# Optimization experiments

Measured on AMD Instinct MI355X. Metric: run time of the kernel, lower is better.

## Reference

```python
import jax, jax.numpy as jnp
import numpy as np

N, E, E_D, EN_D, H = 50000, 200000, 16, 64, 32


def setup_inputs() -> dict:
    key = jax.random.key(0)
    ks = jax.random.split(key, 12)
    x = jax.random.normal(ks[0], (N, H), dtype=jnp.float32)
    edge_data = jax.random.normal(ks[1], (E, E_D), dtype=jnp.float32)
    edges = jax.random.randint(ks[2], (E, 2), 0, N, dtype=jnp.int32)
    # edge_net params: Linear(e_d->en_d), Linear(en_d->h*h)
    W1 = jax.random.normal(ks[3], (EN_D, E_D), dtype=jnp.float32) / np.sqrt(E_D)
    b1 = jax.random.normal(ks[4], (EN_D,), dtype=jnp.float32) * 0.01
    W2 = jax.random.normal(ks[5], (H * H, EN_D), dtype=jnp.float32) / np.sqrt(EN_D)
    b2 = jax.random.normal(ks[6], (H * H,), dtype=jnp.float32) * 0.01
    # GRUCell(input=2*h, hidden=h) params (torch layout: [3h, in], gates r,z,n)
    W_ih = jax.random.normal(ks[7], (3 * H, 2 * H), dtype=jnp.float32) / np.sqrt(2 * H)
    W_hh = jax.random.normal(ks[8], (3 * H, H), dtype=jnp.float32) / np.sqrt(H)
    b_ih = jax.random.normal(ks[9], (3 * H,), dtype=jnp.float32) * 0.01
    b_hh = jax.random.normal(ks[10], (3 * H,), dtype=jnp.float32) * 0.01
    return {"x": x, "edge_data": edge_data, "edges": edges, "T": 8,
            "W1": W1, "b1": b1, "W2": W2, "b2": b2,
            "W_ih": W_ih, "W_hh": W_hh, "b_ih": b_ih, "b_hh": b_hh}


def _gru_cell(inp, h, W_ih, W_hh, b_ih, b_hh):
    gi = inp @ W_ih.T + b_ih   # [N, 3h]
    gh = h @ W_hh.T + b_hh     # [N, 3h]
    i_r, i_z, i_n = jnp.split(gi, 3, axis=1)
    h_r, h_z, h_n = jnp.split(gh, 3, axis=1)
    r = jax.nn.sigmoid(i_r + h_r)
    z = jax.nn.sigmoid(i_z + h_z)
    n = jnp.tanh(i_n + r * h_n)
    return (1.0 - z) * n + z * h


def reference(x, edge_data, edges, T, W1, b1, W2, b2, W_ih, W_hh, b_ih, b_hh):
    h = x.shape[1]
    # per-edge message matrices A_e = edge_net(edge_data_e): [E, h, h]
    hid = jax.nn.relu(edge_data @ W1.T + b1)
    A = jax.nn.relu(hid @ W2.T + b2).reshape(-1, h, h)
    src, dst = edges[:, 0], edges[:, 1]
    # message src is ALWAYS edges[e,0]; message added to both endpoints,
    # only once when src == dst (faithful to the v/e_id loop in the original).
    not_self = (src != dst)[:, None].astype(x.dtype)
    for _ in range(T):
        msg = jnp.einsum('eij,ej->ei', A, x[src])            # [E, h]
        m = jnp.zeros_like(x).at[src].add(msg).at[dst].add(msg * not_self)
        x = _gru_cell(jnp.concatenate([x, m], axis=1), x, W_ih, W_hh, b_ih, b_hh)
    return x
```

## Files before the change

### kernel.cpp

```cpp
#include <hip/hip_runtime.h>
#include <stdint.h>

#define N_NODES 50000
#define N_EDGES 200000
#define H 32
#define T_STEPS 8
#define NGROUPS (N_EDGES / 64)
#define SCAN_B 196

typedef __attribute__((ext_vector_type(4))) float v4f;
typedef __attribute__((ext_vector_type(8))) _Float16 h8;

#define LO_SCALE 4096.0f
#define LO_DESCALE 2.44140625e-4f

__device__ __forceinline__ uint32_t packh2(_Float16 a, _Float16 b) {
  return (uint32_t)__builtin_bit_cast(unsigned short, a) |
         ((uint32_t)__builtin_bit_cast(unsigned short, b) << 16);
}

__global__ void w1pack_kernel(const float* __restrict__ W1, float* __restrict__ W1P) {
  int o = threadIdx.x + blockIdx.x * blockDim.x;
  int d = o >> 4, k = o & 15;
  W1P[k * 64 + d] = W1[o];
}

__global__ void hidb_kernel(const float* __restrict__ ed, const float* __restrict__ W1P,
                            const float* __restrict__ b1,
                            uint32_t* __restrict__ hidh, uint32_t* __restrict__ hidl) {
  int idx = blockIdx.x * blockDim.x + threadIdx.x;
  int e = idx >> 5, d2 = idx & 31;
  int d0 = d2 * 2;
  const float4* er = (const float4*)(ed + (size_t)e * 16);
  float2 bb = *(const float2*)(b1 + d0);
  float a0 = bb.x, a1 = bb.y;
#pragma unroll
  for (int k = 0; k < 4; k++) {
    float4 h = er[k];
    float2 w0 = *(const float2*)(W1P + (4 * k + 0) * 64 + d0);
    float2 w1 = *(const float2*)(W1P + (4 * k + 1) * 64 + d0);
    float2 w2 = *(const float2*)(W1P + (4 * k + 2) * 64 + d0);
    float2 w3 = *(const float2*)(W1P + (4 * k + 3) * 64 + d0);
    a0 += h.x * w0.x + h.y * w1.x + h.z * w2.x + h.w * w3.x;
    a1 += h.x * w0.y + h.y * w1.y + h.z * w2.y + h.w * w3.y;
  }
  a0 = fmaxf(a0, 0.f);
  a1 = fmaxf(a1, 0.f);
  _Float16 h0 = (_Float16)a0, h1 = (_Float16)a1;
  _Float16 l0 = (_Float16)((a0 - (float)h0) * LO_SCALE);
  _Float16 l1 = (_Float16)((a1 - (float)h1) * LO_SCALE);
  hidh[idx] = packh2(h0, h1);
  hidl[idx] = packh2(l0, l1);
}

__global__ void w2pack_kernel(const float* __restrict__ W2,
                              uint32_t* __restrict__ W2Fh, uint32_t* __restrict__ W2Fl) {
  int o = blockIdx.x * blockDim.x + threadIdx.x;
  int c = o >> 8, u = o & 255;
  int lane = u >> 2, pr = u & 3;
  int mtg = c >> 1, kh = c & 1;
  int row = mtg * 16 + (lane & 15);
  int k = kh * 32 + (lane >> 4) * 8 + pr * 2;
  float v0 = W2[(size_t)row * 64 + k];
  float v1 = W2[(size_t)row * 64 + k + 1];
  _Float16 h0 = (_Float16)v0, h1 = (_Float16)v1;
  _Float16 l0 = (_Float16)((v0 - (float)h0) * LO_SCALE);
  _Float16 l1 = (_Float16)((v1 - (float)h1) * LO_SCALE);
  W2Fh[o] = packh2(h0, h1);
  W2Fl[o] = packh2(l0, l1);
}

__global__ void zero_cur_kernel(int* __restrict__ cur) {
  int i = blockIdx.x * blockDim.x + threadIdx.x;
  if (i < N_NODES) cur[i] = 0;
}
__global__ void count_kernel(const int* __restrict__ edges, int* __restrict__ cur) {
  int e = blockIdx.x * blockDim.x + threadIdx.x;
  if (e < N_EDGES) {
    int s = edges[2 * e], d = edges[2 * e + 1];
    atomicAdd(&cur[s], 1);
    if (d != s) atomicAdd(&cur[d], 1);
  }
}
__global__ __launch_bounds__(256) void bsum_kernel(const int* __restrict__ cur,
                                                   int* __restrict__ bsum) {
  __shared__ int s[256];
  int b = blockIdx.x, t = threadIdx.x;
  int idx = b * 256 + t;
  s[t] = (idx < N_NODES) ? cur[idx] : 0;
  __syncthreads();
  for (int d = 128; d > 0; d >>= 1) {
    if (t < d) s[t] += s[t + d];
    __syncthreads();
  }
  if (t == 0) bsum[b] = s[0];
}
__global__ __launch_bounds__(256) void bscan_kernel(const int* __restrict__ bsum,
                                                    int* __restrict__ bbase,
                                                    int* __restrict__ off) {
  __shared__ int s[256];
  int t = threadIdx.x;
  int v = (t < SCAN_B) ? bsum[t] : 0;
  s[t] = v;
  __syncthreads();
  for (int d = 1; d < 256; d <<= 1) {
    int u = (t >= d) ? s[t - d] : 0;
    __syncthreads();
    s[t] += u;
    __syncthreads();
  }
  if (t < SCAN_B) bbase[t] = s[t] - v;
  if (t == SCAN_B - 1) off[N_NODES] = s[t];
}
__global__ __launch_bounds__(256) void boff_kernel(const int* __restrict__ bbase,
                                                   int* __restrict__ cur,
                                                   int* __restrict__ off) {
  __shared__ int s[256];
  int b = blockIdx.x, t = threadIdx.x;
  int idx = b * 256 + t;
  int v = (idx < N_NODES) ? cur[idx] : 0;
  s[t] = v;
  __syncthreads();
  for (int d = 1; d < 256; d <<= 1) {
    int u = (t >= d) ? s[t - d] : 0;
    __syncthreads();
    s[t] += u;
    __syncthreads();
  }
  if (idx < N_NODES) {
    int ex = bbase[b] + s[t] - v;
    off[idx] = ex;
    cur[idx] = ex;
  }
}
__global__ void scatter_kernel(const int* __restrict__ edges, int* __restrict__ cur,
                               int* __restrict__ inc) {
  int e = blockIdx.x * blockDim.x + threadIdx.x;
  if (e < N_EDGES) {
    int s = edges[2 * e], d = edges[2 * e + 1];
    int p = atomicAdd(&cur[s], 1);
    inc[p] = e;
    if (d != s) {
      p = atomicAdd(&cur[d], 1);
      inc[p] = e;
    }
  }
}

typedef __attribute__((address_space(1))) const uint32_t gq_u32;
typedef __attribute__((address_space(3))) uint32_t lds_q_u32;
__device__ __forceinline__ void gload_lds16(const uint32_t* g, uint32_t* l) {
  __builtin_amdgcn_global_load_lds((gq_u32*)g, (lds_q_u32*)l, 16, 0, 0);
}

__device__ __forceinline__ void stage_eighth(const uint32_t* __restrict__ W2Fh,
                                             const uint32_t* __restrict__ W2Fl,
                                             uint32_t* bh, uint32_t* bl,
                                             int eighth, int wv, int lane) {
#pragma unroll
  for (int k = 0; k < 4; k++) {
    int ub = (wv * 4 + k) * 256;
    int u  = ub + lane * 4;
    gload_lds16(W2Fh + eighth * 4096 + u, bh + ub);
    gload_lds16(W2Fl + eighth * 4096 + u, bl + ub);
  }
}

template <int NS>
__device__ __forceinline__ void do_pass(
    const uint32_t* __restrict__ W2Fh, const uint32_t* __restrict__ W2Fl,
    uint32_t (*w2h)[4096], uint32_t (*w2l)[4096], const float* b2s,
    const h8 (&bh0)[NS], const h8 (&bh1)[NS],
    const h8 (&bl0)[NS], const h8 (&bl1)[NS],
    const v4f (&xv0)[NS], const v4f (&xv1)[NS], const int (&ee)[NS],
    float* __restrict__ msg, int wv, int lane, int kg, bool last) {
  int cb = 0;
  for (int s = 0; s < 8; ++s) {
    if (!(last && s == 7)) {
      stage_eighth(W2Fh, W2Fl, w2h[cb ^ 1], w2l[cb ^ 1], (s + 1) & 7, wv, lane);
    }
    int q = s >> 1, h = s & 1;
    const h8* sh = (const h8*)w2h[cb];
    const h8* sl = (const h8*)w2l[cb];
    const float* b2p = b2s + q * 256 + h * 128 + kg * 4;

    float sacc[NS][4];
#pragma unroll
    for (int mp2 = 0; mp2 < 4; mp2++) {
      float tacc[NS];
#pragma unroll
      for (int u = 0; u < NS; u++) tacc[u] = 0.f;
#pragma unroll
      for (int tp = 0; tp < 2; tp++) {
        int lm = 2 * mp2 + tp;
        h8 ah0 = sh[(size_t)(lm * 2 + 0) * 64 + lane];
        h8 ah1 = sh[(size_t)(lm * 2 + 1) * 64 + lane];
        h8 al0 = sl[(size_t)(lm * 2 + 0) * 64 + lane];
        h8 al1 = sl[(size_t)(lm * 2 + 1) * 64 + lane];
        v4f bias = *(const v4f*)(b2p + lm * 16);
#pragma unroll
        for (int u = 0; u < NS; u++) {
          v4f chi = bias;
          chi = __builtin_amdgcn_mfma_f32_16x16x32_f16(ah0, bh0[u], chi, 0, 0, 0);
          chi = __builtin_amdgcn_mfma_f32_16x16x32_f16(ah1, bh1[u], chi, 0, 0, 0);
          v4f clo = {0.f, 0.f, 0.f, 0.f};
          clo = __builtin_amdgcn_mfma_f32_16x16x32_f16(ah0, bl0[u], clo, 0, 0, 0);
          clo = __builtin_amdgcn_mfma_f32_16x16x32_f16(ah1, bl1[u], clo, 0, 0, 0);
          clo = __builtin_amdgcn_mfma_f32_16x16x32_f16(al0, bh0[u], clo, 0, 0, 0);
          clo = __builtin_amdgcn_mfma_f32_16x16x32_f16(al1, bh1[u], clo, 0, 0, 0);
          v4f xr = tp ? xv1[u] : xv0[u];
#pragma unroll
          for (int r = 0; r < 4; r++) {
            float av = fmaxf(fmaf(clo[r], LO_DESCALE, chi[r]), 0.f);
            tacc[u] = fmaf(av, xr[r], tacc[u]);
          }
        }
      }
#pragma unroll
      for (int u = 0; u < NS; u++) {
        float sv = tacc[u];
        sv += __shfl_xor(sv, 16, 64);
        sv += __shfl_xor(sv, 32, 64);
        sacc[u][mp2] = sv;
      }
    }
    if (lane < 16) {
#pragma unroll
      for (int u = 0; u < NS; u++) {
        v4f sv4 = {sacc[u][0], sacc[u][1], sacc[u][2], sacc[u][3]};
        *(v4f*)(msg + (size_t)ee[u] * 32 + q * 8 + h * 4) = sv4;
      }
    }
    __syncthreads();
    cb ^= 1;
  }
}

template <int NS>
__device__ __forceinline__ void load_sets(
    const uint32_t* __restrict__ hidh, const uint32_t* __restrict__ hidl,
    const float* __restrict__ x, const int* __restrict__ edges,
    int gbase, int wv, int el, int kg,
    h8 (&bh0)[NS], h8 (&bh1)[NS], h8 (&bl0)[NS], h8 (&bl1)[NS],
    v4f (&xv0)[NS], v4f (&xv1)[NS], int (&ee)[NS]) {
  const h8* hbh = (const h8*)hidh;
  const h8* hbl = (const h8*)hidl;
#pragma unroll
  for (int u = 0; u < NS; u++) {
    int e = (gbase + u) * 64 + wv * 16 + el;
    ee[u] = e;
    int src = edges[2 * e];
    bh0[u] = hbh[(size_t)e * 8 + kg];
    bh1[u] = hbh[(size_t)e * 8 + 4 + kg];
    bl0[u] = hbl[(size_t)e * 8 + kg];
    bl1[u] = hbl[(size_t)e * 8 + 4 + kg];
    xv0[u] = *(const v4f*)(x + (size_t)src * 32 + kg * 4);
    xv1[u] = *(const v4f*)(x + (size_t)src * 32 + 16 + kg * 4);
  }
}

__global__ __launch_bounds__(256, 2) void msg_kernel(
    const uint32_t* __restrict__ W2Fh, const uint32_t* __restrict__ W2Fl,
    const uint32_t* __restrict__ hidh, const uint32_t* __restrict__ hidl,
    const float* __restrict__ b2, const float* __restrict__ x,
    const int* __restrict__ edges, float* __restrict__ msg) {
  __shared__ uint32_t w2h[2][4096];
  __shared__ uint32_t w2l[2][4096];
  __shared__ float b2s[1024];
  int t = threadIdx.x;
  int bid = blockIdx.x;
  int gs = (int)(((long)bid * NGROUPS) >> 9);
  int ge = (int)(((long)(bid + 1) * NGROUPS) >> 9);
  int n = ge - gs;
  int wv = t >> 6, lane = t & 63;
  int el = lane & 15, kg = lane >> 4;

  for (int i = t; i < 1024; i += 256) b2s[i] = b2[i];
  stage_eighth(W2Fh, W2Fl, w2h[0], w2l[0], 0, wv, lane);

  h8 bh0[4], bh1[4], bl0[4], bl1[4];
  v4f xv0[4], xv1[4];
  int ee[4];
  load_sets<4>(hidh, hidl, x, edges, gs, wv, el, kg,
               bh0, bh1, bl0, bl1, xv0, xv1, ee);
  __syncthreads();

  do_pass<4>(W2Fh, W2Fl, w2h, w2l, b2s, bh0, bh1, bl0, bl1, xv0, xv1, ee,
             msg, wv, lane, kg, false);

  __builtin_amdgcn_sched_barrier(0);

  if (n == 6) {
    h8 cbh0[2], cbh1[2], cbl0[2], cbl1[2];
    v4f cxv0[2], cxv1[2];
    int cee[2];
    load_sets<2>(hidh, hidl, x, edges, gs + 4, wv, el, kg,
                 cbh0, cbh1, cbl0, cbl1, cxv0, cxv1, cee);
    do_pass<2>(W2Fh, W2Fl, w2h, w2l, b2s, cbh0, cbh1, cbl0, cbl1,
               cxv0, cxv1, cee, msg, wv, lane, kg, true);
  } else {
    h8 cbh0[3], cbh1[3], cbl0[3], cbl1[3];
    v4f cxv0[3], cxv1[3];
    int cee[3];
    load_sets<3>(hidh, hidl, x, edges, gs + 4, wv, el, kg,
                 cbh0, cbh1, cbl0, cbl1, cxv0, cxv1, cee);
    do_pass<3>(W2Fh, W2Fl, w2h, w2l, b2s, cbh0, cbh1, cbl0, cbl1,
               cxv0, cxv1, cee, msg, wv, lane, kg, true);
  }
}

__global__ __launch_bounds__(512) void node_kernel(
    float* __restrict__ x, const float* __restrict__ msg,
    const int* __restrict__ off, const int* __restrict__ inc,
    const float* __restrict__ W_ih, const float* __restrict__ W_hh,
    const float* __restrict__ b_ih, const float* __restrict__ b_hh) {
  __shared__ float wih[64 * 97];
  __shared__ float whh[32 * 97];
  __shared__ float xs[16][32], ms[16][32];
  int t = threadIdx.x;
  for (int p = t; p < 6144; p += 512) {
    int q = p >> 6, k = p & 63;
    wih[k * 97 + q] = W_ih[p];
  }
  for (int p = t; p < 3072; p += 512) {
    int q = p >> 5, k = p & 31;
    whh[k * 97 + q] = W_hh[p];
  }
  int slot = t >> 5, i = t & 31;
  int n = blockIdx.x * 16 + slot;
  float xv = x[(size_t)n * 32 + i];
  xs[slot][i] = xv;
  const float* msgq = msg + i;
  int s0 = off[n], s1 = off[n + 1];
  float a0 = 0.f, a1 = 0.f, a2 = 0.f, a3 = 0.f;
  float a4 = 0.f, a5 = 0.f, a6 = 0.f, a7 = 0.f;
  int k = s0;
  for (; k + 8 <= s1; k += 8) {
    int e0 = inc[k],     e1 = inc[k + 1], e2 = inc[k + 2], e3 = inc[k + 3];
    int e4 = inc[k + 4], e5 = inc[k + 5], e6 = inc[k + 6], e7 = inc[k + 7];
    a0 += msgq[(size_t)e0 * 32];
    a1 += msgq[(size_t)e1 * 32];
    a2 += msgq[(size_t)e2 * 32];
    a3 += msgq[(size_t)e3 * 32];
    a4 += msgq[(size_t)e4 * 32];
    a5 += msgq[(size_t)e5 * 32];
    a6 += msgq[(size_t)e6 * 32];
    a7 += msgq[(size_t)e7 * 32];
  }
  if (k + 4 <= s1) {
    int e0 = inc[k], e1 = inc[k + 1], e2 = inc[k + 2], e3 = inc[k + 3];
    a0 += msgq[(size_t)e0 * 32];
    a1 += msgq[(size_t)e1 * 32];
    a2 += msgq[(size_t)e2 * 32];
    a3 += msgq[(size_t)e3 * 32];
    k += 4;
  }
  for (; k < s1; k++) a0 += msgq[(size_t)inc[k] * 32];
  ms[slot][i] = ((a0 + a1) + (a2 + a3)) + ((a4 + a5) + (a6 + a7));
  __syncthreads();

  float gir = b_ih[i], giz = b_ih[32 + i], gin = b_ih[64 + i];
  float ghr = b_hh[i], ghz = b_hh[32 + i], ghn = b_hh[64 + i];
#pragma unroll 4
  for (int kk = 0; kk < 32; kk++) {
    float xk = xs[slot][kk];
    float mk = ms[slot][kk];
    const float* wa = &wih[kk * 97];
    const float* wb = &wih[(32 + kk) * 97];
    gir += xk * wa[i] + mk * wb[i];
    giz += xk * wa[32 + i] + mk * wb[32 + i];
    gin += xk * wa[64 + i] + mk * wb[64 + i];
    const float* hc = &whh[kk * 97];
    ghr += xk * hc[i];
    ghz += xk * hc[32 + i];
    ghn += xk * hc[64 + i];
  }
  float r = 1.f / (1.f + __expf(-(gir + ghr)));
  float z = 1.f / (1.f + __expf(-(giz + ghz)));
  float nn = tanhf(gin + r * ghn);
  x[(size_t)n * 32 + i] = (1.f - z) * nn + z * xv;
}

__global__ void copy4_kernel(float4* __restrict__ dst, const float4* __restrict__ src, int n4) {
  int i = blockIdx.x * blockDim.x + threadIdx.x;
  if (i < n4) dst[i] = src[i];
}

extern "C" void kernel_launch(void* const* d_in, const int* in_sizes, int n_in,
                              void* d_out, int out_size, void* d_ws, size_t ws_size,
                              hipStream_t stream) {
  const float* x_in      = (const float*)d_in[0];
  const float* edge_data = (const float*)d_in[1];
  const int*   edges     = (const int*)d_in[2];
  const float* W1   = (const float*)d_in[4];
  const float* b1   = (const float*)d_in[5];
  const float* W2   = (const float*)d_in[6];
  const float* b2   = (const float*)d_in[7];
  const float* W_ih = (const float*)d_in[8];
  const float* W_hh = (const float*)d_in[9];
  const float* b_ih = (const float*)d_in[10];
  const float* b_hh = (const float*)d_in[11];

  char* ws = (char*)d_ws;
  size_t o = 0;
  uint32_t* hidh = (uint32_t*)(ws + o); o += (size_t)N_EDGES * 64 * 2;
  uint32_t* hidl = (uint32_t*)(ws + o); o += (size_t)N_EDGES * 64 * 2;
  uint32_t* W2Fh = (uint32_t*)(ws + o); o += 32768u * 4;
  uint32_t* W2Fl = (uint32_t*)(ws + o); o += 32768u * 4;
  float*    W1P  = (float*)(ws + o);    o += 1024u * 4;
  int*      inc  = (int*)(ws + o);      o += (size_t)2 * N_EDGES * 4;
  int*      off  = (int*)(ws + o);      o += (size_t)(N_NODES + 4) * 4;
  int*      cur  = (int*)(ws + o);      o += (size_t)N_NODES * 4;
  int*      bsum = (int*)(ws + o);      o += (size_t)256 * 4;
  int*      bbase= (int*)(ws + o);      o += (size_t)256 * 4;
  float*    msg  = (float*)(ws + o);    o += (size_t)N_EDGES * 32 * 4;
  float*    x    = (float*)d_out;

  const int n4x = N_NODES * H / 4;
  copy4_kernel<<<(n4x + 255) / 256, 256, 0, stream>>>((float4*)x, (const float4*)x_in, n4x);
  w1pack_kernel<<<4, 256, 0, stream>>>(W1, W1P);
  hidb_kernel<<<N_EDGES * 32 / 256, 256, 0, stream>>>(edge_data, W1P, b1, hidh, hidl);
  w2pack_kernel<<<32768 / 256, 256, 0, stream>>>(W2, W2Fh, W2Fl);

  zero_cur_kernel<<<(N_NODES + 255) / 256, 256, 0, stream>>>(cur);
  count_kernel<<<(N_EDGES + 255) / 256, 256, 0, stream>>>(edges, cur);
  bsum_kernel<<<SCAN_B, 256, 0, stream>>>(cur, bsum);
  bscan_kernel<<<1, 256, 0, stream>>>(bsum, bbase, off);
  boff_kernel<<<SCAN_B, 256, 0, stream>>>(bbase, cur, off);
  scatter_kernel<<<(N_EDGES + 255) / 256, 256, 0, stream>>>(edges, cur, inc);

  for (int it = 0; it < T_STEPS; it++) {
    msg_kernel<<<512, 256, 0, stream>>>(W2Fh, W2Fl, hidh, hidl, b2, x, edges, msg);
    node_kernel<<<N_NODES / 16, 512, 0, stream>>>(x, msg, off, inc,
                                                  W_ih, W_hh, b_ih, b_hh);
  }
}
```

Measured before the change: 1.347 ms.

## Double msg_kernel grid and stage W2 in sixteenths with smaller LDS buffers

The message kernel now launches 1024 blocks instead of 512, so each block handles 3-4 edge groups in a single pass rather than two passes over 6-7 groups. The W2 weight staging is split into 16 smaller chunks, which halves the LDS double buffers. The first half of each output quad is held in registers until the second half is computed. The aim is more blocks, better occupancy and better load balance across CUs, at the cost of re-streaming the full W2 matrix once per block (twice as many total W2 reads) and twice as many barriers per pass.

```diff
diff --git a/kernel.cpp b/kernel.cpp
--- a/kernel.cpp
+++ b/kernel.cpp
@@ -7,6 +7,7 @@
 #define T_STEPS 8
 #define NGROUPS (N_EDGES / 64)
 #define SCAN_B 196
+#define MSG_GRID 1024
 
 typedef __attribute__((ext_vector_type(4))) float v4f;
 typedef __attribute__((ext_vector_type(8))) _Float16 h8;
@@ -153,51 +154,52 @@
   __builtin_amdgcn_global_load_lds((gq_u32*)g, (lds_q_u32*)l, 16, 0, 0);
 }
 
-__device__ __forceinline__ void stage_eighth(const uint32_t* __restrict__ W2Fh,
-                                             const uint32_t* __restrict__ W2Fl,
-                                             uint32_t* bh, uint32_t* bl,
-                                             int eighth, int wv, int lane) {
-#pragma unroll
-  for (int k = 0; k < 4; k++) {
-    int ub = (wv * 4 + k) * 256;
+__device__ __forceinline__ void stage_16th(const uint32_t* __restrict__ W2Fh,
+                                           const uint32_t* __restrict__ W2Fl,
+                                           uint32_t* bh, uint32_t* bl,
+                                           int s16, int wv, int lane) {
+#pragma unroll
+  for (int k = 0; k < 2; k++) {
+    int ub = (wv * 2 + k) * 256;
     int u  = ub + lane * 4;
-    gload_lds16(W2Fh + eighth * 4096 + u, bh + ub);
-    gload_lds16(W2Fl + eighth * 4096 + u, bl + ub);
+    gload_lds16(W2Fh + s16 * 2048 + u, bh + ub);
+    gload_lds16(W2Fl + s16 * 2048 + u, bl + ub);
   }
 }
 
 template <int NS>
 __device__ __forceinline__ void do_pass(
     const uint32_t* __restrict__ W2Fh, const uint32_t* __restrict__ W2Fl,
-    uint32_t (*w2h)[4096], uint32_t (*w2l)[4096], const float* b2s,
+    uint32_t (*w2h)[2048], uint32_t (*w2l)[2048], const float* b2s,
     const h8 (&bh0)[NS], const h8 (&bh1)[NS],
     const h8 (&bl0)[NS], const h8 (&bl1)[NS],
     const v4f (&xv0)[NS], const v4f (&xv1)[NS], const int (&ee)[NS],
-    float* __restrict__ msg, int wv, int lane, int kg, bool last) {
+    float* __restrict__ msg, int wv, int lane, int kg) {
   int cb = 0;
-  for (int s = 0; s < 8; ++s) {
-    if (!(last && s == 7)) {
-      stage_eighth(W2Fh, W2Fl, w2h[cb ^ 1], w2l[cb ^ 1], (s + 1) & 7, wv, lane);
+  float hold[NS][2];
+  for (int s = 0; s < 16; ++s) {
+    if (s < 15) {
+      stage_16th(W2Fh, W2Fl, w2h[cb ^ 1], w2l[cb ^ 1], s + 1, wv, lane);
     }
-    int q = s >> 1, h = s & 1;
+    int q = s >> 2, h = (s >> 1) & 1, half = s & 1;
     const h8* sh = (const h8*)w2h[cb];
     const h8* sl = (const h8*)w2l[cb];
-    const float* b2p = b2s + q * 256 + h * 128 + kg * 4;
-
-    float sacc[NS][4];
-#pragma unroll
-    for (int mp2 = 0; mp2 < 4; mp2++) {
+
+    float sacc[NS][2];
+#pragma unroll
+    for (int mp2 = 0; mp2 < 2; mp2++) {
       float tacc[NS];
 #pragma unroll
       for (int u = 0; u < NS; u++) tacc[u] = 0.f;
 #pragma unroll
       for (int tp = 0; tp < 2; tp++) {
-        int lm = 2 * mp2 + tp;
-        h8 ah0 = sh[(size_t)(lm * 2 + 0) * 64 + lane];
-        h8 ah1 = sh[(size_t)(lm * 2 + 1) * 64 + lane];
-        h8 al0 = sl[(size_t)(lm * 2 + 0) * 64 + lane];
-        h8 al1 = sl[(size_t)(lm * 2 + 1) * 64 + lane];
-        v4f bias = *(const v4f*)(b2p + lm * 16);
+        int lml = 2 * mp2 + tp;
+        h8 ah0 = sh[(size_t)(lml * 2 + 0) * 64 + lane];
+        h8 ah1 = sh[(size_t)(lml * 2 + 1) * 64 + lane];
+        h8 al0 = sl[(size_t)(lml * 2 + 0) * 64 + lane];
+        h8 al1 = sl[(size_t)(lml * 2 + 1) * 64 + lane];
+        int lm = half * 4 + lml;
+        v4f bias = *(const v4f*)(b2s + q * 256 + h * 128 + lm * 16 + kg * 4);
 #pragma unroll
         for (int u = 0; u < NS; u++) {
           v4f chi = bias;
@@ -224,10 +226,16 @@
         sacc[u][mp2] = sv;
       }
     }
-    if (lane < 16) {
+    if (half == 0) {
 #pragma unroll
       for (int u = 0; u < NS; u++) {
-        v4f sv4 = {sacc[u][0], sacc[u][1], sacc[u][2], sacc[u][3]};
+        hold[u][0] = sacc[u][0];
+        hold[u][1] = sacc[u][1];
+      }
+    } else if (lane < 16) {
+#pragma unroll
+      for (int u = 0; u < NS; u++) {
+        v4f sv4 = {hold[u][0], hold[u][1], sacc[u][0], sacc[u][1]};
         *(v4f*)(msg + (size_t)ee[u] * 32 + q * 8 + h * 4) = sv4;
       }
     }
@@ -264,48 +272,38 @@
     const uint32_t* __restrict__ hidh, const uint32_t* __restrict__ hidl,
     const float* __restrict__ b2, const float* __restrict__ x,
     const int* __restrict__ edges, float* __restrict__ msg) {
-  __shared__ uint32_t w2h[2][4096];
-  __shared__ uint32_t w2l[2][4096];
+  __shared__ uint32_t w2h[2][2048];
+  __shared__ uint32_t w2l[2][2048];
   __shared__ float b2s[1024];
   int t = threadIdx.x;
   int bid = blockIdx.x;
-  int gs = (int)(((long)bid * NGROUPS) >> 9);
-  int ge = (int)(((long)(bid + 1) * NGROUPS) >> 9);
+  int gs = (int)(((long)bid * NGROUPS) >> 10);
+  int ge = (int)(((long)(bid + 1) * NGROUPS) >> 10);
   int n = ge - gs;
   int wv = t >> 6, lane = t & 63;
   int el = lane & 15, kg = lane >> 4;
 
   for (int i = t; i < 1024; i += 256) b2s[i] = b2[i];
-  stage_eighth(W2Fh, W2Fl, w2h[0], w2l[0], 0, wv, lane);
-
-  h8 bh0[4], bh1[4], bl0[4], bl1[4];
-  v4f xv0[4], xv1[4];
-  int ee[4];
-  load_sets<4>(hidh, hidl, x, edges, gs, wv, el, kg,
-               bh0, bh1, bl0, bl1, xv0, xv1, ee);
-  __syncthreads();
-
-  do_pass<4>(W2Fh, W2Fl, w2h, w2l, b2s, bh0, bh1, bl0, bl1, xv0, xv1, ee,
-             msg, wv, lane, kg, false);
-
-  __builtin_amdgcn_sched_barrier(0);
-
-  if (n == 6) {
-    h8 cbh0[2], cbh1[2], cbl0[2], cbl1[2];
-    v4f cxv0[2], cxv1[2];
-    int cee[2];
-    load_sets<2>(hidh, hidl, x, edges, gs + 4, wv, el, kg,
-                 cbh0, cbh1, cbl0, cbl1, cxv0, cxv1, cee);
-    do_pass<2>(W2Fh, W2Fl, w2h, w2l, b2s, cbh0, cbh1, cbl0, cbl1,
-               cxv0, cxv1, cee, msg, wv, lane, kg, true);
+  stage_16th(W2Fh, W2Fl, w2h[0], w2l[0], 0, wv, lane);
+
+  if (n == 4) {
+    h8 bh0[4], bh1[4], bl0[4], bl1[4];
+    v4f xv0[4], xv1[4];
+    int ee[4];
+    load_sets<4>(hidh, hidl, x, edges, gs, wv, el, kg,
+                 bh0, bh1, bl0, bl1, xv0, xv1, ee);
+    __syncthreads();
+    do_pass<4>(W2Fh, W2Fl, w2h, w2l, b2s, bh0, bh1, bl0, bl1, xv0, xv1, ee,
+               msg, wv, lane, kg);
   } else {
-    h8 cbh0[3], cbh1[3], cbl0[3], cbl1[3];
-    v4f cxv0[3], cxv1[3];
-    int cee[3];
-    load_sets<3>(hidh, hidl, x, edges, gs + 4, wv, el, kg,
-                 cbh0, cbh1, cbl0, cbl1, cxv0, cxv1, cee);
-    do_pass<3>(W2Fh, W2Fl, w2h, w2l, b2s, cbh0, cbh1, cbl0, cbl1,
-               cxv0, cxv1, cee, msg, wv, lane, kg, true);
+    h8 bh0[3], bh1[3], bl0[3], bl1[3];
+    v4f xv0[3], xv1[3];
+    int ee[3];
+    load_sets<3>(hidh, hidl, x, edges, gs, wv, el, kg,
+                 bh0, bh1, bl0, bl1, xv0, xv1, ee);
+    __syncthreads();
+    do_pass<3>(W2Fh, W2Fl, w2h, w2l, b2s, bh0, bh1, bl0, bl1, xv0, xv1, ee,
+               msg, wv, lane, kg);
   }
 }
 
@@ -430,7 +428,7 @@
   scatter_kernel<<<(N_EDGES + 255) / 256, 256, 0, stream>>>(edges, cur, inc);
 
   for (int it = 0; it < T_STEPS; it++) {
-    msg_kernel<<<512, 256, 0, stream>>>(W2Fh, W2Fl, hidh, hidl, b2, x, edges, msg);
+    msg_kernel<<<MSG_GRID, 256, 0, stream>>>(W2Fh, W2Fl, hidh, hidl, b2, x, edges, msg);
     node_kernel<<<N_NODES / 16, 512, 0, stream>>>(x, msg, off, inc,
                                                   W_ih, W_hh, b_ih, b_hh);
   }
```

Result: slower. 1.421 ms (+5.5%).
